# Kernel tuning notes

Measured on AMD Instinct MI355X. Metric: run time of the kernel, lower is better.

Reference implementation:

```python
import jax, jax.numpy as jnp
import numpy as np

N = 768       # num nodes
E = 12288     # num edges (avg degree 16)
D_IN = 6
H = 256       # hidden_dim
TEMPERATURE = 1.0


def gcn_conv(x, W, b, src, dst, n):
    """PyG GCNConv: add self-loops, symmetric deg^-1/2 normalization, then xW aggregation + bias."""
    h = x @ W  # [n, H]
    loop = jnp.arange(n, dtype=src.dtype)
    s = jnp.concatenate([src, loop])
    d = jnp.concatenate([dst, loop])
    deg = jax.ops.segment_sum(jnp.ones(s.shape, dtype=h.dtype), d, num_segments=n)
    dinv = jnp.where(deg > 0, jax.lax.rsqrt(deg), 0.0)
    norm = dinv[s] * dinv[d]  # [E+n]
    out = jax.ops.segment_sum(h[s] * norm[:, None], d, num_segments=n)
    return out + b


def setup_inputs() -> dict:
    key = jax.random.key(0)
    ks = jax.random.split(key, 10)
    sc = lambda fan: np.float32(1.0 / np.sqrt(fan))
    x = jax.random.normal(ks[0], (N, D_IN), jnp.float32)
    edge_index = jax.random.randint(ks[1], (2, E), 0, N, dtype=jnp.int32)
    Wc1 = jax.random.normal(ks[2], (D_IN, H), jnp.float32) * sc(D_IN)
    bc1 = jnp.zeros((H,), jnp.float32)
    Wc2 = jax.random.normal(ks[3], (H, H), jnp.float32) * sc(H)
    bc2 = jnp.zeros((H,), jnp.float32)
    We1 = jax.random.normal(ks[4], (2 * H, H), jnp.float32) * sc(2 * H)
    be1 = jax.random.normal(ks[5], (H,), jnp.float32) * sc(2 * H)
    We2 = jax.random.normal(ks[6], (H, 1), jnp.float32) * sc(H)
    be2 = jax.random.normal(ks[7], (1,), jnp.float32) * sc(H)
    return {"x": x, "edge_index": edge_index, "Wc1": Wc1, "bc1": bc1,
            "Wc2": Wc2, "bc2": bc2, "We1": We1, "be1": be1, "We2": We2, "be2": be2}


def reference(x, edge_index, Wc1, bc1, Wc2, bc2, We1, be1, We2, be2):
    src, dst = edge_index[0], edge_index[1]
    h = jax.nn.elu(gcn_conv(x, Wc1, bc1, src, dst, N))
    h = gcn_conv(h, Wc2, bc2, src, dst, N)  # [N, H]
    # edge scorer: Linear(cat([x_i, x_j])) == x_i @ We1[:H] + x_j @ We1[H:] + be1
    ai = h @ We1[:H]   # [N, H], contribution of x_i (row node)
    aj = h @ We1[H:]   # [N, H], contribution of x_j (col node)
    pair = jax.nn.relu(ai[:, None, :] + aj[None, :, :] + be1)  # [N, N, H]
    logits = jnp.einsum('ijh,h->ij', pair, We2[:, 0]) + be2[0]  # [N, N]
    logits = logits / TEMPERATURE
    logits = jnp.where(jnp.eye(N, dtype=bool), -jnp.inf, logits)
    return jax.nn.softmax(logits, axis=-1)
```

## Files before the change

kernel.cpp:

```cpp
#include <hip/hip_runtime.h>
#include <math.h>

#define N_NODES 768
#define N_EDGES 12288
#define D_INF 6
#define H 256
#define H2 512
#define CAP 128
#define LC 256
#define SA 260

__global__ __launch_bounds__(256) void k_front(
    const float* __restrict__ x, const int* __restrict__ ei,
    const float* __restrict__ Wc1, const float* __restrict__ bc1,
    const float* __restrict__ Wc2, const float* __restrict__ bc2,
    const float* __restrict__ We1, const float* __restrict__ be1,
    int* __restrict__ cnt_g, int* __restrict__ slots,
    float* __restrict__ h1, float* __restrict__ Wcombo, float* __restrict__ bias_c)
{
    const int t = threadIdx.x;
    if (blockIdx.x < 256) {
        __shared__ int s_cnt[N_NODES];
        __shared__ int s_list[LC];
        __shared__ int s_nm;
        __shared__ int s_pos[3];
        __shared__ float s_agg[3][D_INF];
        const int b = blockIdx.x, v0 = b * 3;
        const int* src = ei;
        const int* dst = ei + N_EDGES;
        for (int v = t; v < N_NODES; v += 256) s_cnt[v] = 0;
        if (t == 0) s_nm = 0;
        if (t < 3) s_pos[t] = 0;
        if (t < 3 * D_INF) ((float*)s_agg)[t] = 0.f;
        __syncthreads();
        for (int e = t; e < N_EDGES; e += 256) {
            int d = dst[e];
            atomicAdd(&s_cnt[d], 1);
            unsigned li = (unsigned)(d - v0);
            if (li < 3u) {
                int s = src[e];
                int p = atomicAdd(&s_nm, 1);
                if (p < LC) s_list[p] = (s << 2) | (int)li;
            }
        }
        __syncthreads();
        const int nm = min(s_nm, LC);
        if (t < 3) cnt_g[v0 + t] = s_cnt[v0 + t];
        for (int m = t; m < nm; m += 256) {
            int pk = s_list[m];
            int s = pk >> 2, li = pk & 3;
            int p = atomicAdd(&s_pos[li], 1);
            if (p < CAP) slots[(v0 + li) * CAP + p] = s;
            float w = rsqrtf((float)(s_cnt[s] + 1)) * rsqrtf((float)(s_cnt[v0 + li] + 1));
            #pragma unroll
            for (int k = 0; k < D_INF; ++k)
                atomicAdd(&s_agg[li][k], w * x[s * D_INF + k]);
        }
        if (t < 3) {
            int v = v0 + t;
            float dv2 = 1.0f / (float)(s_cnt[v] + 1);
            #pragma unroll
            for (int k = 0; k < D_INF; ++k)
                atomicAdd(&s_agg[t][k], dv2 * x[v * D_INF + k]);
        }
        __syncthreads();
        #pragma unroll
        for (int r = 0; r < 3; ++r) {
            float acc = bc1[t];
            #pragma unroll
            for (int k = 0; k < D_INF; ++k)
                acc = fmaf(s_agg[r][k], Wc1[k * H + t], acc);
            h1[(v0 + r) * H + t] = (acc > 0.f) ? acc : expm1f(acc);
        }
    } else {
        __shared__ __align__(16) float s_a[32 * SA];
        __shared__ __align__(16) float s_bT[16 * SA];
        __shared__ float s_bc2[H];
        const int idx = blockIdx.x - 256;
        const int rg = idx >> 5, cp = idx & 31;
        const int r0 = rg * 32, c0 = cp * 16;
        const int c = t & 15, ro = t >> 4;
        for (int i = t; i < 32 * 64; i += 256) {
            int r = i >> 6, q = i & 63;
            float4 v = *(const float4*)(Wc2 + (size_t)(r0 + r) * H + q * 4);
            *(float4*)&s_a[r * SA + q * 4] = v;
        }
        {
            int kk = t >> 4, cc = t & 15;
            int cg = c0 + cc;
            const float* Wsrc = (cg < H) ? (We1 + cg)
                                         : (We1 + (size_t)H * H + (cg - H));
            #pragma unroll
            for (int it = 0; it < 16; ++it) {
                int k = kk + it * 16;
                s_bT[cc * SA + k] = Wsrc[(size_t)k * H];
            }
        }
        s_bc2[t] = bc2[t];
        __syncthreads();
        float a0 = 0.f, a1 = 0.f;
        #pragma unroll 8
        for (int kg = 0; kg < 64; ++kg) {
            float4 w  = *(const float4*)&s_bT[c * SA + kg * 4];
            float4 v0 = *(const float4*)&s_a[(ro)      * SA + kg * 4];
            float4 v1 = *(const float4*)&s_a[(ro + 16) * SA + kg * 4];
            a0 = fmaf(v0.x, w.x, a0); a0 = fmaf(v0.y, w.y, a0);
            a0 = fmaf(v0.z, w.z, a0); a0 = fmaf(v0.w, w.w, a0);
            a1 = fmaf(v1.x, w.x, a1); a1 = fmaf(v1.y, w.y, a1);
            a1 = fmaf(v1.z, w.z, a1); a1 = fmaf(v1.w, w.w, a1);
        }
        Wcombo[(size_t)(r0 + ro)      * H2 + c0 + c] = a0;
        Wcombo[(size_t)(r0 + ro + 16) * H2 + c0 + c] = a1;
        if (rg == 0 && t < 16) {
            int cg = c0 + t;
            float bias = (cg >= H) ? be1[cg - H] : 0.f;
            for (int k = 0; k < H; ++k)
                bias = fmaf(s_bc2[k], s_bT[t * SA + k], bias);
            bias_c[cg] = bias;
        }
    }
}

__global__ __launch_bounds__(256) void k_agg(
    const float* __restrict__ h1, const int* __restrict__ cnt,
    const int* __restrict__ slots, float* __restrict__ agg2) {
    __shared__ int   s_s[CAP];
    __shared__ float s_w[CAP];
    const int v = blockIdx.x, t = threadIdx.x;
    const int c = cnt[v];
    const int cc = min(c, CAP);
    const float dv = rsqrtf((float)(c + 1));
    for (int i = t; i < cc; i += 256) {
        int s = slots[v * CAP + i];
        s_s[i] = s;
        s_w[i] = rsqrtf((float)(cnt[s] + 1)) * dv;
    }
    __syncthreads();
    float acc = dv * dv * h1[v * H + t];
    #pragma unroll 4
    for (int n = 0; n < cc; ++n)
        acc = fmaf(s_w[n], h1[s_s[n] * H + t], acc);
    agg2[v * H + t] = acc;
}

__global__ __launch_bounds__(256) void k_ae2(
    const float* __restrict__ agg2, const float* __restrict__ Wcombo,
    const float* __restrict__ bias_c, float* __restrict__ aib,
    float* __restrict__ ajcT) {
    __shared__ __align__(16) float s_h[32 * SA];
    __shared__ __align__(16) float s_wT[16 * SA];
    const int t = threadIdx.x, b = blockIdx.x;
    const int rg = b >> 5, cp = b & 31;
    const int j0 = rg * 32, c0 = cp * 16;
    const int c = t & 15, ro = t >> 4;

    for (int i = t; i < 32 * 64; i += 256) {
        int r = i >> 6, q = i & 63;
        float4 v = *(const float4*)(agg2 + (size_t)(j0 + r) * H + q * 4);
        *(float4*)&s_h[r * SA + q * 4] = v;
    }
    {
        int kk = t >> 4, cc = t & 15;
        #pragma unroll
        for (int it = 0; it < 16; ++it) {
            int k = kk + it * 16;
            s_wT[cc * SA + k] = Wcombo[(size_t)k * H2 + c0 + cc];
        }
    }
    __syncthreads();

    float pa0 = 0.f, pa1 = 0.f;
    #pragma unroll 8
    for (int kg = 0; kg < 64; ++kg) {
        float4 w  = *(const float4*)&s_wT[c * SA + kg * 4];
        float4 v0 = *(const float4*)&s_h[(ro)      * SA + kg * 4];
        float4 v1 = *(const float4*)&s_h[(ro + 16) * SA + kg * 4];
        pa0 = fmaf(v0.x, w.x, pa0); pa0 = fmaf(v0.y, w.y, pa0);
        pa0 = fmaf(v0.z, w.z, pa0); pa0 = fmaf(v0.w, w.w, pa0);
        pa1 = fmaf(v1.x, w.x, pa1); pa1 = fmaf(v1.y, w.y, pa1);
        pa1 = fmaf(v1.z, w.z, pa1); pa1 = fmaf(v1.w, w.w, pa1);
    }
    int cg = c0 + c;
    float bb = bias_c[cg];
    if (cg < H) {
        aib[(size_t)(j0 + ro)      * H + cg] = pa0 + bb;
        aib[(size_t)(j0 + ro + 16) * H + cg] = pa1 + bb;
    } else {
        ajcT[(size_t)(cg - H) * N_NODES + j0 + ro]      = pa0 + bb;
        ajcT[(size_t)(cg - H) * N_NODES + j0 + ro + 16] = pa1 + bb;
    }
}

__global__ __launch_bounds__(512) void k_pairA(
    const float* __restrict__ aib, const float* __restrict__ ajcT,
    const float* __restrict__ We2, float* __restrict__ logits_p) {
    __shared__ float s_ai[12 * H];
    __shared__ float s_w2[H];
    const int t = threadIdx.x, b = blockIdx.x;
    const int tc = t & 255, th = t >> 8;
    const int rg = b >> 2, hp = b & 3;
    const int i0 = rg * 12, h0 = hp * 64;

    for (int i = t; i < 12 * H; i += 512) {
        int r = i >> 8, col = i & 255;
        s_ai[r * H + col] = aib[(size_t)(i0 + r) * H + col];
    }
    if (t < H) s_w2[t] = We2[t];
    __syncthreads();

    const int r0 = th * 6;
    float acc[6][3];
    #pragma unroll
    for (int r = 0; r < 6; ++r)
        #pragma unroll
        for (int jj = 0; jj < 3; ++jj) acc[r][jj] = 0.f;

    #pragma unroll 4
    for (int hh = 0; hh < 64; ++hh) {
        int h = h0 + hh;
        float wv = s_w2[h];
        const float* col = ajcT + (size_t)h * N_NODES;
        float b0 = col[tc], b1 = col[tc + 256], b2 = col[tc + 512];
        #pragma unroll
        for (int r = 0; r < 6; ++r) {
            float av = s_ai[(r0 + r) * H + h];
            acc[r][0] = fmaf(fmaxf(av + b0, 0.f), wv, acc[r][0]);
            acc[r][1] = fmaf(fmaxf(av + b1, 0.f), wv, acc[r][1]);
            acc[r][2] = fmaf(fmaxf(av + b2, 0.f), wv, acc[r][2]);
        }
    }
    #pragma unroll
    for (int r = 0; r < 6; ++r) {
        float* row = logits_p + ((size_t)hp * N_NODES + i0 + r0 + r) * N_NODES;
        #pragma unroll
        for (int jj = 0; jj < 3; ++jj)
            row[tc + jj * 256] = acc[r][jj];
    }
}

__global__ __launch_bounds__(256) void k_soft(
    const float* __restrict__ logits_p, float* __restrict__ out) {
    __shared__ float red[256];
    const int i = blockIdx.x, t = threadIdx.x;
    float l[3];
    #pragma unroll
    for (int jj = 0; jj < 3; ++jj) {
        int j = t + jj * 256;
        float s = 0.f;
        #pragma unroll
        for (int hp = 0; hp < 4; ++hp)
            s += logits_p[((size_t)hp * N_NODES + i) * N_NODES + j];
        l[jj] = (j == i) ? -INFINITY : s;
    }
    red[t] = fmaxf(fmaxf(l[0], l[1]), l[2]);
    __syncthreads();
    for (int s = 128; s > 0; s >>= 1) {
        if (t < s) red[t] = fmaxf(red[t], red[t + s]);
        __syncthreads();
    }
    float mx = red[0];
    __syncthreads();
    float e0 = __expf(l[0] - mx), e1 = __expf(l[1] - mx), e2 = __expf(l[2] - mx);
    red[t] = e0 + e1 + e2;
    __syncthreads();
    for (int s = 128; s > 0; s >>= 1) {
        if (t < s) red[t] += red[t + s];
        __syncthreads();
    }
    float inv = 1.0f / red[0];
    out[(size_t)i * N_NODES + t]       = e0 * inv;
    out[(size_t)i * N_NODES + t + 256] = e1 * inv;
    out[(size_t)i * N_NODES + t + 512] = e2 * inv;
}

extern "C" void kernel_launch(void* const* d_in, const int* in_sizes, int n_in,
                              void* d_out, int out_size, void* d_ws, size_t ws_size,
                              hipStream_t stream) {
    const float* x   = (const float*)d_in[0];
    const int*   ei  = (const int*)d_in[1];
    const float* Wc1 = (const float*)d_in[2];
    const float* bc1 = (const float*)d_in[3];
    const float* Wc2 = (const float*)d_in[4];
    const float* bc2 = (const float*)d_in[5];
    const float* We1 = (const float*)d_in[6];
    const float* be1 = (const float*)d_in[7];
    const float* We2 = (const float*)d_in[8];
    float* out = (float*)d_out;

    char* ws = (char*)d_ws;
    int*   cnt      = (int*)(ws + 0);
    int*   slots    = (int*)(ws + 4096);
    float* h1       = (float*)(ws + 397312);
    float* agg2     = (float*)(ws + 1183744);
    float* aib      = (float*)(ws + 1970176);
    float* ajcT     = (float*)(ws + 2756608);
    float* Wcombo   = (float*)(ws + 3543040);
    float* bias_c   = (float*)(ws + 4067328);
    float* logits_p = (float*)(ws + 4069376);

    k_front<<<512, 256, 0, stream>>>(x, ei, Wc1, bc1, Wc2, bc2, We1, be1,
                                     cnt, slots, h1, Wcombo, bias_c);
    k_agg<<<N_NODES, 256, 0, stream>>>(h1, cnt, slots, agg2);
    k_ae2<<<768, 256, 0, stream>>>(agg2, Wcombo, bias_c, aib, ajcT);
    k_pairA<<<256, 512, 0, stream>>>(aib, ajcT, We2, logits_p);
    k_soft<<<N_NODES, 256, 0, stream>>>(logits_p, out);
}
```

Baseline: 57.30 us.

## Unfold weight precombination, fuse pair scorer with softmax, restructure GEMMs

Drops the precomputed Wc2·We1 combined weight and instead computes h2 = agg2·Wc2 and then ai/aj in two separate 1024-thread split-K kernels that reduce partials in shared memory. The pair-scoring kernel now handles 3 rows per block across all hidden units and performs the diagonal mask and softmax in-block, so the partial-logits buffer and the separate softmax kernel go away. This removes a global round trip of the logits and one launch, but adds an extra GEMM launch, runs the pair stage on only 256 blocks with large shared memory, and reads weights directly from global memory per block.

Result: faster. 54.68 us (-4.6%).

```diff
diff --git a/kernel.cpp b/kernel.cpp
--- a/kernel.cpp
+++ b/kernel.cpp
@@ -5,119 +5,63 @@
 #define N_EDGES 12288
 #define D_INF 6
 #define H 256
-#define H2 512
 #define CAP 128
 #define LC 256
-#define SA 260
-
-__global__ __launch_bounds__(256) void k_front(
+
+__global__ __launch_bounds__(256) void k_prep(
     const float* __restrict__ x, const int* __restrict__ ei,
     const float* __restrict__ Wc1, const float* __restrict__ bc1,
-    const float* __restrict__ Wc2, const float* __restrict__ bc2,
-    const float* __restrict__ We1, const float* __restrict__ be1,
-    int* __restrict__ cnt_g, int* __restrict__ slots,
-    float* __restrict__ h1, float* __restrict__ Wcombo, float* __restrict__ bias_c)
-{
-    const int t = threadIdx.x;
-    if (blockIdx.x < 256) {
-        __shared__ int s_cnt[N_NODES];
-        __shared__ int s_list[LC];
-        __shared__ int s_nm;
-        __shared__ int s_pos[3];
-        __shared__ float s_agg[3][D_INF];
-        const int b = blockIdx.x, v0 = b * 3;
-        const int* src = ei;
-        const int* dst = ei + N_EDGES;
-        for (int v = t; v < N_NODES; v += 256) s_cnt[v] = 0;
-        if (t == 0) s_nm = 0;
-        if (t < 3) s_pos[t] = 0;
-        if (t < 3 * D_INF) ((float*)s_agg)[t] = 0.f;
-        __syncthreads();
-        for (int e = t; e < N_EDGES; e += 256) {
-            int d = dst[e];
-            atomicAdd(&s_cnt[d], 1);
-            unsigned li = (unsigned)(d - v0);
-            if (li < 3u) {
-                int s = src[e];
-                int p = atomicAdd(&s_nm, 1);
-                if (p < LC) s_list[p] = (s << 2) | (int)li;
-            }
-        }
-        __syncthreads();
-        const int nm = min(s_nm, LC);
-        if (t < 3) cnt_g[v0 + t] = s_cnt[v0 + t];
-        for (int m = t; m < nm; m += 256) {
-            int pk = s_list[m];
-            int s = pk >> 2, li = pk & 3;
-            int p = atomicAdd(&s_pos[li], 1);
-            if (p < CAP) slots[(v0 + li) * CAP + p] = s;
-            float w = rsqrtf((float)(s_cnt[s] + 1)) * rsqrtf((float)(s_cnt[v0 + li] + 1));
-            #pragma unroll
-            for (int k = 0; k < D_INF; ++k)
-                atomicAdd(&s_agg[li][k], w * x[s * D_INF + k]);
-        }
-        if (t < 3) {
-            int v = v0 + t;
-            float dv2 = 1.0f / (float)(s_cnt[v] + 1);
-            #pragma unroll
-            for (int k = 0; k < D_INF; ++k)
-                atomicAdd(&s_agg[t][k], dv2 * x[v * D_INF + k]);
-        }
-        __syncthreads();
-        #pragma unroll
-        for (int r = 0; r < 3; ++r) {
-            float acc = bc1[t];
-            #pragma unroll
-            for (int k = 0; k < D_INF; ++k)
-                acc = fmaf(s_agg[r][k], Wc1[k * H + t], acc);
-            h1[(v0 + r) * H + t] = (acc > 0.f) ? acc : expm1f(acc);
-        }
-    } else {
-        __shared__ __align__(16) float s_a[32 * SA];
-        __shared__ __align__(16) float s_bT[16 * SA];
-        __shared__ float s_bc2[H];
-        const int idx = blockIdx.x - 256;
-        const int rg = idx >> 5, cp = idx & 31;
-        const int r0 = rg * 32, c0 = cp * 16;
-        const int c = t & 15, ro = t >> 4;
-        for (int i = t; i < 32 * 64; i += 256) {
-            int r = i >> 6, q = i & 63;
-            float4 v = *(const float4*)(Wc2 + (size_t)(r0 + r) * H + q * 4);
-            *(float4*)&s_a[r * SA + q * 4] = v;
-        }
-        {
-            int kk = t >> 4, cc = t & 15;
-            int cg = c0 + cc;
-            const float* Wsrc = (cg < H) ? (We1 + cg)
-                                         : (We1 + (size_t)H * H + (cg - H));
-            #pragma unroll
-            for (int it = 0; it < 16; ++it) {
-                int k = kk + it * 16;
-                s_bT[cc * SA + k] = Wsrc[(size_t)k * H];
-            }
-        }
-        s_bc2[t] = bc2[t];
-        __syncthreads();
-        float a0 = 0.f, a1 = 0.f;
-        #pragma unroll 8
-        for (int kg = 0; kg < 64; ++kg) {
-            float4 w  = *(const float4*)&s_bT[c * SA + kg * 4];
-            float4 v0 = *(const float4*)&s_a[(ro)      * SA + kg * 4];
-            float4 v1 = *(const float4*)&s_a[(ro + 16) * SA + kg * 4];
-            a0 = fmaf(v0.x, w.x, a0); a0 = fmaf(v0.y, w.y, a0);
-            a0 = fmaf(v0.z, w.z, a0); a0 = fmaf(v0.w, w.w, a0);
-            a1 = fmaf(v1.x, w.x, a1); a1 = fmaf(v1.y, w.y, a1);
-            a1 = fmaf(v1.z, w.z, a1); a1 = fmaf(v1.w, w.w, a1);
-        }
-        Wcombo[(size_t)(r0 + ro)      * H2 + c0 + c] = a0;
-        Wcombo[(size_t)(r0 + ro + 16) * H2 + c0 + c] = a1;
-        if (rg == 0 && t < 16) {
-            int cg = c0 + t;
-            float bias = (cg >= H) ? be1[cg - H] : 0.f;
-            for (int k = 0; k < H; ++k)
-                bias = fmaf(s_bc2[k], s_bT[t * SA + k], bias);
-            bias_c[cg] = bias;
-        }
+    int* __restrict__ cnt_g, int* __restrict__ slots, float* __restrict__ h1) {
+    __shared__ int s_cnt[N_NODES];
+    __shared__ int s_list[LC];
+    __shared__ int s_nm, s_pos[3];
+    __shared__ float s_agg[3][D_INF];
+    const int t = threadIdx.x, b = blockIdx.x, v0 = b * 3;
+    const int* src = ei;
+    const int* dst = ei + N_EDGES;
+
+    for (int v = t; v < N_NODES; v += 256) s_cnt[v] = 0;
+    if (t == 0) s_nm = 0;
+    if (t < 3) s_pos[t] = 0;
+    if (t < 3 * D_INF) ((float*)s_agg)[t] = 0.f;
+    __syncthreads();
+    for (int e = t; e < N_EDGES; e += 256) {
+        int d = dst[e];
+        atomicAdd(&s_cnt[d], 1);
+        unsigned li = (unsigned)(d - v0);
+        if (li < 3u) {
+            int p = atomicAdd(&s_nm, 1);
+            if (p < LC) s_list[p] = (src[e] << 2) | (int)li;
+        }
+    }
+    __syncthreads();
+    const int nm = min(s_nm, LC);
+    if (t < 3) cnt_g[v0 + t] = s_cnt[v0 + t];
+    for (int m = t; m < nm; m += 256) {
+        int pk = s_list[m];
+        int s = pk >> 2, li = pk & 3;
+        int p = atomicAdd(&s_pos[li], 1);
+        if (p < CAP) slots[(v0 + li) * CAP + p] = s;
+        float w = rsqrtf((float)(s_cnt[s] + 1)) * rsqrtf((float)(s_cnt[v0 + li] + 1));
+        #pragma unroll
+        for (int k = 0; k < D_INF; ++k)
+            atomicAdd(&s_agg[li][k], w * x[s * D_INF + k]);
+    }
+    if (t < 3) {
+        int v = v0 + t;
+        float dv2 = 1.0f / (float)(s_cnt[v] + 1);
+        #pragma unroll
+        for (int k = 0; k < D_INF; ++k)
+            atomicAdd(&s_agg[t][k], dv2 * x[v * D_INF + k]);
+    }
+    __syncthreads();
+    #pragma unroll
+    for (int r = 0; r < 3; ++r) {
+        float acc = bc1[t];
+        #pragma unroll
+        for (int k = 0; k < D_INF; ++k)
+            acc = fmaf(s_agg[r][k], Wc1[k * H + t], acc);
+        h1[(v0 + r) * H + t] = (acc > 0.f) ? acc : expm1f(acc);
     }
 }
 
@@ -143,134 +87,213 @@
     agg2[v * H + t] = acc;
 }
 
-__global__ __launch_bounds__(256) void k_ae2(
-    const float* __restrict__ agg2, const float* __restrict__ Wcombo,
-    const float* __restrict__ bias_c, float* __restrict__ aib,
+__global__ __launch_bounds__(1024) void k_h2(
+    const float* __restrict__ agg2, const float* __restrict__ Wc2,
+    const float* __restrict__ bc2, float* __restrict__ h2) {
+    __shared__ __align__(16) float s_part[16][3][H];
+    const int t = threadIdx.x, b = blockIdx.x;
+    const int lane = t & 63, w = t >> 6;
+    const int v0 = b * 3, k0 = w * 16;
+
+    float a[3][16];
+    #pragma unroll
+    for (int r = 0; r < 3; ++r)
+        #pragma unroll
+        for (int q = 0; q < 4; ++q) {
+            float4 v = *(const float4*)(agg2 + (size_t)(v0 + r) * H + k0 + q * 4);
+            a[r][q * 4 + 0] = v.x; a[r][q * 4 + 1] = v.y;
+            a[r][q * 4 + 2] = v.z; a[r][q * 4 + 3] = v.w;
+        }
+    float4 c0 = {0.f, 0.f, 0.f, 0.f}, c1 = c0, c2 = c0;
+    #pragma unroll
+    for (int kk = 0; kk < 16; ++kk) {
+        float4 wv = *(const float4*)(Wc2 + (size_t)(k0 + kk) * H + (lane << 2));
+        c0.x = fmaf(a[0][kk], wv.x, c0.x); c0.y = fmaf(a[0][kk], wv.y, c0.y);
+        c0.z = fmaf(a[0][kk], wv.z, c0.z); c0.w = fmaf(a[0][kk], wv.w, c0.w);
+        c1.x = fmaf(a[1][kk], wv.x, c1.x); c1.y = fmaf(a[1][kk], wv.y, c1.y);
+        c1.z = fmaf(a[1][kk], wv.z, c1.z); c1.w = fmaf(a[1][kk], wv.w, c1.w);
+        c2.x = fmaf(a[2][kk], wv.x, c2.x); c2.y = fmaf(a[2][kk], wv.y, c2.y);
+        c2.z = fmaf(a[2][kk], wv.z, c2.z); c2.w = fmaf(a[2][kk], wv.w, c2.w);
+    }
+    *(float4*)&s_part[w][0][lane << 2] = c0;
+    *(float4*)&s_part[w][1][lane << 2] = c1;
+    *(float4*)&s_part[w][2][lane << 2] = c2;
+    __syncthreads();
+    if (t < 3 * H) {
+        int r = t >> 8, c = t & 255;
+        float v = bc2[c];
+        #pragma unroll
+        for (int ww = 0; ww < 16; ++ww) v += s_part[ww][r][c];
+        h2[(size_t)(v0 + r) * H + c] = v;
+    }
+}
+
+__global__ __launch_bounds__(1024) void k_ae(
+    const float* __restrict__ h2, const float* __restrict__ We1,
+    const float* __restrict__ be1, float* __restrict__ aib,
     float* __restrict__ ajcT) {
-    __shared__ __align__(16) float s_h[32 * SA];
-    __shared__ __align__(16) float s_wT[16 * SA];
+    __shared__ __align__(16) float s_part[16][6][H];
     const int t = threadIdx.x, b = blockIdx.x;
-    const int rg = b >> 5, cp = b & 31;
-    const int j0 = rg * 32, c0 = cp * 16;
-    const int c = t & 15, ro = t >> 4;
-
-    for (int i = t; i < 32 * 64; i += 256) {
-        int r = i >> 6, q = i & 63;
-        float4 v = *(const float4*)(agg2 + (size_t)(j0 + r) * H + q * 4);
-        *(float4*)&s_h[r * SA + q * 4] = v;
-    }
-    {
-        int kk = t >> 4, cc = t & 15;
-        #pragma unroll
-        for (int it = 0; it < 16; ++it) {
-            int k = kk + it * 16;
-            s_wT[cc * SA + k] = Wcombo[(size_t)k * H2 + c0 + cc];
-        }
-    }
-    __syncthreads();
-
-    float pa0 = 0.f, pa1 = 0.f;
-    #pragma unroll 8
-    for (int kg = 0; kg < 64; ++kg) {
-        float4 w  = *(const float4*)&s_wT[c * SA + kg * 4];
-        float4 v0 = *(const float4*)&s_h[(ro)      * SA + kg * 4];
-        float4 v1 = *(const float4*)&s_h[(ro + 16) * SA + kg * 4];
-        pa0 = fmaf(v0.x, w.x, pa0); pa0 = fmaf(v0.y, w.y, pa0);
-        pa0 = fmaf(v0.z, w.z, pa0); pa0 = fmaf(v0.w, w.w, pa0);
-        pa1 = fmaf(v1.x, w.x, pa1); pa1 = fmaf(v1.y, w.y, pa1);
-        pa1 = fmaf(v1.z, w.z, pa1); pa1 = fmaf(v1.w, w.w, pa1);
-    }
-    int cg = c0 + c;
-    float bb = bias_c[cg];
-    if (cg < H) {
-        aib[(size_t)(j0 + ro)      * H + cg] = pa0 + bb;
-        aib[(size_t)(j0 + ro + 16) * H + cg] = pa1 + bb;
-    } else {
-        ajcT[(size_t)(cg - H) * N_NODES + j0 + ro]      = pa0 + bb;
-        ajcT[(size_t)(cg - H) * N_NODES + j0 + ro + 16] = pa1 + bb;
-    }
-}
-
-__global__ __launch_bounds__(512) void k_pairA(
+    const int lane = t & 63, w = t >> 6;
+    const int v0 = b * 3, k0 = w * 16;
+
+    float a[3][16];
+    #pragma unroll
+    for (int r = 0; r < 3; ++r)
+        #pragma unroll
+        for (int q = 0; q < 4; ++q) {
+            float4 v = *(const float4*)(h2 + (size_t)(v0 + r) * H + k0 + q * 4);
+            a[r][q * 4 + 0] = v.x; a[r][q * 4 + 1] = v.y;
+            a[r][q * 4 + 2] = v.z; a[r][q * 4 + 3] = v.w;
+        }
+    float4 ca0 = {0.f, 0.f, 0.f, 0.f}, ca1 = ca0, ca2 = ca0;
+    float4 cb0 = ca0, cb1 = ca0, cb2 = ca0;
+    #pragma unroll
+    for (int kk = 0; kk < 16; ++kk) {
+        int k = k0 + kk;
+        float4 wa = *(const float4*)(We1 + (size_t)k * H + (lane << 2));
+        float4 wb = *(const float4*)(We1 + (size_t)(H + k) * H + (lane << 2));
+        ca0.x = fmaf(a[0][kk], wa.x, ca0.x); ca0.y = fmaf(a[0][kk], wa.y, ca0.y);
+        ca0.z = fmaf(a[0][kk], wa.z, ca0.z); ca0.w = fmaf(a[0][kk], wa.w, ca0.w);
+        ca1.x = fmaf(a[1][kk], wa.x, ca1.x); ca1.y = fmaf(a[1][kk], wa.y, ca1.y);
+        ca1.z = fmaf(a[1][kk], wa.z, ca1.z); ca1.w = fmaf(a[1][kk], wa.w, ca1.w);
+        ca2.x = fmaf(a[2][kk], wa.x, ca2.x); ca2.y = fmaf(a[2][kk], wa.y, ca2.y);
+        ca2.z = fmaf(a[2][kk], wa.z, ca2.z); ca2.w = fmaf(a[2][kk], wa.w, ca2.w);
+        cb0.x = fmaf(a[0][kk], wb.x, cb0.x); cb0.y = fmaf(a[0][kk], wb.y, cb0.y);
+        cb0.z = fmaf(a[0][kk], wb.z, cb0.z); cb0.w = fmaf(a[0][kk], wb.w, cb0.w);
+        cb1.x = fmaf(a[1][kk], wb.x, cb1.x); cb1.y = fmaf(a[1][kk], wb.y, cb1.y);
+        cb1.z = fmaf(a[1][kk], wb.z, cb1.z); cb1.w = fmaf(a[1][kk], wb.w, cb1.w);
+        cb2.x = fmaf(a[2][kk], wb.x, cb2.x); cb2.y = fmaf(a[2][kk], wb.y, cb2.y);
+        cb2.z = fmaf(a[2][kk], wb.z, cb2.z); cb2.w = fmaf(a[2][kk], wb.w, cb2.w);
+    }
+    *(float4*)&s_part[w][0][lane << 2] = ca0;
+    *(float4*)&s_part[w][1][lane << 2] = ca1;
+    *(float4*)&s_part[w][2][lane << 2] = ca2;
+    *(float4*)&s_part[w][3][lane << 2] = cb0;
+    *(float4*)&s_part[w][4][lane << 2] = cb1;
+    *(float4*)&s_part[w][5][lane << 2] = cb2;
+    __syncthreads();
+    for (int idx = t; idx < 6 * H; idx += 1024) {
+        int q = idx >> 8, c = idx & 255;
+        float v = 0.f;
+        #pragma unroll
+        for (int ww = 0; ww < 16; ++ww) v += s_part[ww][q][c];
+        if (q < 3) aib[(size_t)(v0 + q) * H + c] = v;
+        else       ajcT[(size_t)c * N_NODES + v0 + (q - 3)] = v + be1[c];
+    }
+}
+
+__global__ __launch_bounds__(512) void k_pair2(
     const float* __restrict__ aib, const float* __restrict__ ajcT,
-    const float* __restrict__ We2, float* __restrict__ logits_p) {
-    __shared__ float s_ai[12 * H];
+    const float* __restrict__ We2, float* __restrict__ out) {
+    __shared__ float s_ai[3 * H];
     __shared__ float s_w2[H];
+    __shared__ __align__(16) float s_p[8 * 3 * N_NODES];
+    __shared__ float s_lg[3 * N_NODES];
+    __shared__ float red[3 * 256];
     const int t = threadIdx.x, b = blockIdx.x;
-    const int tc = t & 255, th = t >> 8;
-    const int rg = b >> 2, hp = b & 3;
-    const int i0 = rg * 12, h0 = hp * 64;
-
-    for (int i = t; i < 12 * H; i += 512) {
-        int r = i >> 8, col = i & 255;
-        s_ai[r * H + col] = aib[(size_t)(i0 + r) * H + col];
-    }
+    const int lane = t & 63, w = t >> 6;
+    const int i0 = b * 3, h0 = w * 32;
+
+    for (int i = t; i < 3 * H; i += 512)
+        s_ai[i] = aib[(size_t)(i0 + (i >> 8)) * H + (i & 255)];
     if (t < H) s_w2[t] = We2[t];
     __syncthreads();
 
-    const int r0 = th * 6;
-    float acc[6][3];
-    #pragma unroll
-    for (int r = 0; r < 6; ++r)
-        #pragma unroll
-        for (int jj = 0; jj < 3; ++jj) acc[r][jj] = 0.f;
+    float4 acc[3][3];
+    #pragma unroll
+    for (int r = 0; r < 3; ++r)
+        #pragma unroll
+        for (int jj = 0; jj < 3; ++jj)
+            acc[r][jj] = make_float4(0.f, 0.f, 0.f, 0.f);
 
     #pragma unroll 4
-    for (int hh = 0; hh < 64; ++hh) {
+    for (int hh = 0; hh < 32; ++hh) {
         int h = h0 + hh;
         float wv = s_w2[h];
-        const float* col = ajcT + (size_t)h * N_NODES;
-        float b0 = col[tc], b1 = col[tc + 256], b2 = col[tc + 512];
-        #pragma unroll
-        for (int r = 0; r < 6; ++r) {
-            float av = s_ai[(r0 + r) * H + h];
-            acc[r][0] = fmaf(fmaxf(av + b0, 0.f), wv, acc[r][0]);
-            acc[r][1] = fmaf(fmaxf(av + b1, 0.f), wv, acc[r][1]);
-            acc[r][2] = fmaf(fmaxf(av + b2, 0.f), wv, acc[r][2]);
-        }
-    }
-    #pragma unroll
-    for (int r = 0; r < 6; ++r) {
-        float* row = logits_p + ((size_t)hp * N_NODES + i0 + r0 + r) * N_NODES;
+        float a0 = s_ai[h], a1 = s_ai[H + h], a2 = s_ai[2 * H + h];
+        const float* col = ajcT + (size_t)h * N_NODES + (lane << 2);
+        #pragma unroll
+        for (int jj = 0; jj < 3; ++jj) {
+            float4 bv = *(const float4*)(col + jj * 256);
+            acc[0][jj].x = fmaf(fmaxf(a0 + bv.x, 0.f), wv, acc[0][jj].x);
+            acc[0][jj].y = fmaf(fmaxf(a0 + bv.y, 0.f), wv, acc[0][jj].y);
+            acc[0][jj].z = fmaf(fmaxf(a0 + bv.z, 0.f), wv, acc[0][jj].z);
+            acc[0][jj].w = fmaf(fmaxf(a0 + bv.w, 0.f), wv, acc[0][jj].w);
+            acc[1][jj].x = fmaf(fmaxf(a1 + bv.x, 0.f), wv, acc[1][jj].x);
+            acc[1][jj].y = fmaf(fmaxf(a1 + bv.y, 0.f), wv, acc[1][jj].y);
+            acc[1][jj].z = fmaf(fmaxf(a1 + bv.z, 0.f), wv, acc[1][jj].z);
+            acc[1][jj].w = fmaf(fmaxf(a1 + bv.w, 0.f), wv, acc[1][jj].w);
+            acc[2][jj].x = fmaf(fmaxf(a2 + bv.x, 0.f), wv, acc[2][jj].x);
+            acc[2][jj].y = fmaf(fmaxf(a2 + bv.y, 0.f), wv, acc[2][jj].y);
+            acc[2][jj].z = fmaf(fmaxf(a2 + bv.z, 0.f), wv, acc[2][jj].z);
+            acc[2][jj].w = fmaf(fmaxf(a2 + bv.w, 0.f), wv, acc[2][jj].w);
+        }
+    }
+    #pragma unroll
+    for (int r = 0; r < 3; ++r)
         #pragma unroll
         for (int jj = 0; jj < 3; ++jj)
-            row[tc + jj * 256] = acc[r][jj];
-    }
-}
-
-__global__ __launch_bounds__(256) void k_soft(
-    const float* __restrict__ logits_p, float* __restrict__ out) {
-    __shared__ float red[256];
-    const int i = blockIdx.x, t = threadIdx.x;
-    float l[3];
-    #pragma unroll
-    for (int jj = 0; jj < 3; ++jj) {
-        int j = t + jj * 256;
-        float s = 0.f;
-        #pragma unroll
-        for (int hp = 0; hp < 4; ++hp)
-            s += logits_p[((size_t)hp * N_NODES + i) * N_NODES + j];
-        l[jj] = (j == i) ? -INFINITY : s;
-    }
-    red[t] = fmaxf(fmaxf(l[0], l[1]), l[2]);
+            *(float4*)&s_p[(w * 3 + r) * N_NODES + jj * 256 + (lane << 2)] = acc[r][jj];
+    __syncthreads();
+
+    for (int idx = t; idx < 3 * N_NODES; idx += 512) {
+        int r = idx / N_NODES, j = idx - r * N_NODES;
+        float v = 0.f;
+        #pragma unroll
+        for (int ww = 0; ww < 8; ++ww) v += s_p[(ww * 3 + r) * N_NODES + j];
+        s_lg[idx] = (j == i0 + r) ? -INFINITY : v;
+    }
+    __syncthreads();
+
+    const int tc = t & 255, th = t >> 8;
+    if (th == 0) {
+        red[tc] = fmaxf(fmaxf(s_lg[tc], s_lg[tc + 256]), s_lg[tc + 512]);
+        red[512 + tc] = fmaxf(fmaxf(s_lg[1536 + tc], s_lg[1536 + tc + 256]),
+                              s_lg[1536 + tc + 512]);
+    } else {
+        red[256 + tc] = fmaxf(fmaxf(s_lg[768 + tc], s_lg[768 + tc + 256]),
+                              s_lg[768 + tc + 512]);
+    }
     __syncthreads();
     for (int s = 128; s > 0; s >>= 1) {
-        if (t < s) red[t] = fmaxf(red[t], red[t + s]);
+        if (th == 0 && tc < s) {
+            red[tc] = fmaxf(red[tc], red[tc + s]);
+            red[512 + tc] = fmaxf(red[512 + tc], red[512 + tc + s]);
+        } else if (th == 1 && tc < s) {
+            red[256 + tc] = fmaxf(red[256 + tc], red[256 + tc + s]);
+        }
         __syncthreads();
     }
-    float mx = red[0];
-    __syncthreads();
-    float e0 = __expf(l[0] - mx), e1 = __expf(l[1] - mx), e2 = __expf(l[2] - mx);
-    red[t] = e0 + e1 + e2;
+    float mx0 = red[0], mx1 = red[256], mx2 = red[512];
+    __syncthreads();
+    if (th == 0) {
+        red[tc] = __expf(s_lg[tc] - mx0) + __expf(s_lg[tc + 256] - mx0)
+                + __expf(s_lg[tc + 512] - mx0);
+        red[512 + tc] = __expf(s_lg[1536 + tc] - mx2) + __expf(s_lg[1536 + tc + 256] - mx2)
+                      + __expf(s_lg[1536 + tc + 512] - mx2);
+    } else {
+        red[256 + tc] = __expf(s_lg[768 + tc] - mx1) + __expf(s_lg[768 + tc + 256] - mx1)
+                      + __expf(s_lg[768 + tc + 512] - mx1);
+    }
     __syncthreads();
     for (int s = 128; s > 0; s >>= 1) {
-        if (t < s) red[t] += red[t + s];
+        if (th == 0 && tc < s) {
+            red[tc] += red[tc + s];
+            red[512 + tc] += red[512 + tc + s];
+        } else if (th == 1 && tc < s) {
+            red[256 + tc] += red[256 + tc + s];
+        }
         __syncthreads();
     }
-    float inv = 1.0f / red[0];
-    out[(size_t)i * N_NODES + t]       = e0 * inv;
-    out[(size_t)i * N_NODES + t + 256] = e1 * inv;
-    out[(size_t)i * N_NODES + t + 512] = e2 * inv;
+    float iv0 = 1.0f / red[0], iv1 = 1.0f / red[256], iv2 = 1.0f / red[512];
+
+    for (int idx = t; idx < 3 * N_NODES; idx += 512) {
+        int r = idx / N_NODES, j = idx - r * N_NODES;
+        float m = (r == 0) ? mx0 : (r == 1) ? mx1 : mx2;
+        float iv = (r == 0) ? iv0 : (r == 1) ? iv1 : iv2;
+        out[(size_t)(i0 + r) * N_NODES + j] = __expf(s_lg[idx] - m) * iv;
+    }
 }
 
 extern "C" void kernel_launch(void* const* d_in, const int* in_sizes, int n_in,
@@ -288,20 +311,17 @@
     float* out = (float*)d_out;
 
     char* ws = (char*)d_ws;
-    int*   cnt      = (int*)(ws + 0);
-    int*   slots    = (int*)(ws + 4096);
-    float* h1       = (float*)(ws + 397312);
-    float* agg2     = (float*)(ws + 1183744);
-    float* aib      = (float*)(ws + 1970176);
-    float* ajcT     = (float*)(ws + 2756608);
-    float* Wcombo   = (float*)(ws + 3543040);
-    float* bias_c   = (float*)(ws + 4067328);
-    float* logits_p = (float*)(ws + 4069376);
-
-    k_front<<<512, 256, 0, stream>>>(x, ei, Wc1, bc1, Wc2, bc2, We1, be1,
-                                     cnt, slots, h1, Wcombo, bias_c);
+    int*   cnt  = (int*)(ws + 0);
+    int*   slots= (int*)(ws + 4096);
+    float* h1   = (float*)(ws + 397312);
+    float* agg2 = (float*)(ws + 1183744);
+    float* h2   = (float*)(ws + 1970176);
+    float* aib  = (float*)(ws + 2756608);
+    float* ajcT = (float*)(ws + 3543040);
+
+    k_prep<<<N_NODES / 3, 256, 0, stream>>>(x, ei, Wc1, bc1, cnt, slots, h1);
     k_agg<<<N_NODES, 256, 0, stream>>>(h1, cnt, slots, agg2);
-    k_ae2<<<768, 256, 0, stream>>>(agg2, Wcombo, bias_c, aib, ajcT);
-    k_pairA<<<256, 512, 0, stream>>>(aib, ajcT, We2, logits_p);
-    k_soft<<<N_NODES, 256, 0, stream>>>(logits_p, out);
-}
+    k_h2<<<N_NODES / 3, 1024, 0, stream>>>(agg2, Wc2, bc2, h2);
+    k_ae<<<N_NODES / 3, 1024, 0, stream>>>(h2, We1, be1, aib, ajcT);
+    k_pair2<<<N_NODES / 3, 512, 0, stream>>>(aib, ajcT, We2, out);
+}
```
